# Kernel optimization log

Hardware: AMD Instinct MI355X
Metric: run time of the kernel (lower is better)

The kernel has to match this reference:

```python
import jax, jax.numpy as jnp
import numpy as np

IN_C = 31
OUT_C = 8                      # C: mean/scale channels and Givens rotation size
A_C = OUT_C * (OUT_C - 1) // 2 # 28 rotation angles
TOT = OUT_C + OUT_C + A_C      # encoder output channels = 44
SMIN, SMAX = 0.001, 1000.0
B, H, W = 4, 256, 256


def setup_inputs() -> dict:
    key = jax.random.key(0)
    k1, k2, k3 = jax.random.split(key, 3)
    x = jax.random.normal(k1, (B, IN_C, H, W), dtype=jnp.float32)
    Wenc = jax.random.normal(k2, (TOT, IN_C), dtype=jnp.float32) * (1.0 / np.sqrt(IN_C))
    benc = jax.random.normal(k3, (TOT,), dtype=jnp.float32) * 0.01
    return {"x": x, "Wenc": Wenc, "benc": benc}


def reference(x, Wenc, benc):
    C = OUT_C
    # encoder: 1x1 conv -> (B, TOT, H, W)
    w = jnp.einsum('bchw,oc->bohw', x, Wenc) + benc[None, :, None, None]
    m = jnp.transpose(w[:, :C], (0, 2, 3, 1))                 # (B,H,W,C)
    sig = jax.nn.sigmoid(w[:, C:2 * C])
    s = SMIN * (1.0 - sig) + SMAX * sig                       # (B,C,H,W)
    a = jnp.pi * jnp.tanh(w[:, 2 * C:])                       # (B,A,H,W)
    cs = jnp.cos(a)
    ss = jnp.sin(a)
    # R = prod of Givens rotations; right-multiplying by rij only updates
    # columns i and j, so we never materialize per-pair (B,H,W,C,C) identities.
    eye = jnp.eye(C, dtype=x.dtype)
    R = jnp.broadcast_to(eye, (x.shape[0], x.shape[2], x.shape[3], C, C))
    c = 0
    for i in range(C - 1):
        for j in range(i + 1, C):
            cij = cs[:, c][..., None]   # (B,H,W,1)
            sij = ss[:, c][..., None]
            col_i = R[..., i]           # (B,H,W,C)
            col_j = R[..., j]
            R = R.at[..., i].set(col_i * cij + col_j * sij)
            R = R.at[..., j].set(col_j * cij - col_i * sij)
            c += 1
    sp = jnp.transpose(s, (0, 2, 3, 1))                       # (B,H,W,C)
    # S = R^T D R with D = diag(sp), per pixel
    S = jnp.einsum('bhwji,bhwj,bhwjk->bhwik', R, sp, R)
    S = 0.5 * (S + jnp.swapaxes(S, -1, -2))
    return m, S
```

## Files before the change

kernel.cpp:

```cpp
#include <hip/hip_runtime.h>
#include <math.h>

constexpr int IN_C = 31;
constexpr int TOT  = 44;
constexpr int HW   = 256 * 256;
constexpr int NPIX = 4 * HW;
constexpr float SMIN = 0.001f, SMAX = 1000.0f;

typedef __attribute__((ext_vector_type(8))) short bf16x8;
typedef __attribute__((ext_vector_type(4))) float f32x4;

__device__ __forceinline__ float frcp(float v) { return __builtin_amdgcn_rcpf(v); }

__device__ __forceinline__ short f2bf(float f) {
    union { float f; unsigned u; } v; v.f = f;
    unsigned r = v.u + 0x7FFFu + ((v.u >> 16) & 1u);
    return (short)(r >> 16);
}
__device__ __forceinline__ float bf2f(short h) {
    union { unsigned u; float f; } v; v.u = ((unsigned)(unsigned short)h) << 16;
    return v.f;
}

__global__ __launch_bounds__(64, 4) void sepgpd_fused(
    const float* __restrict__ x,
    const float* __restrict__ Wenc,
    const float* __restrict__ benc,
    float* __restrict__ out)
{
    __shared__ float wt[64 * 34];

    const int lane = threadIdx.x;
    const int W0   = blockIdx.x * 64;
    const int b    = W0 >> 16;
    const int hwb  = W0 & (HW - 1);
    const int lrow = lane & 15;
    const int lgrp = lane >> 4;

    const float* xb = x + (size_t)b * IN_C * HW + hwb;

    bf16x8 bhi[3], blo[3];
#pragma unroll
    for (int n = 0; n < 3; ++n) {
        const int o = n * 16 + lrow;
#pragma unroll
        for (int j = 0; j < 8; ++j) {
            const int k = lgrp * 8 + j;
            const float wv = (o < TOT && k < IN_C) ? Wenc[o * IN_C + k] : 0.0f;
            const short h = f2bf(wv);
            bhi[n][j] = h;
            blo[n][j] = f2bf(wv - bf2f(h));
        }
    }

    f32x4 acc[4][3];
#pragma unroll
    for (int t = 0; t < 4; ++t)
#pragma unroll
        for (int n = 0; n < 3; ++n) acc[t][n] = (f32x4)0.0f;

#pragma unroll
    for (int t = 0; t < 4; ++t) {
        float xf[8];
#pragma unroll
        for (int j = 0; j < 8; ++j) {
            const int k = lgrp * 8 + j;
            xf[j] = (k < IN_C) ? xb[(size_t)k * HW + t * 16 + lrow] : 0.0f;
        }
        bf16x8 ahi, alo;
#pragma unroll
        for (int j = 0; j < 8; ++j) {
            const short h = f2bf(xf[j]);
            ahi[j] = h;
            alo[j] = f2bf(xf[j] - bf2f(h));
        }
#pragma unroll
        for (int n = 0; n < 3; ++n) {
            acc[t][n] = __builtin_amdgcn_mfma_f32_16x16x32_bf16(ahi, bhi[n], acc[t][n], 0, 0, 0);
            acc[t][n] = __builtin_amdgcn_mfma_f32_16x16x32_bf16(alo, bhi[n], acc[t][n], 0, 0, 0);
            acc[t][n] = __builtin_amdgcn_mfma_f32_16x16x32_bf16(ahi, blo[n], acc[t][n], 0, 0, 0);
        }
    }

#pragma unroll
    for (int t = 0; t < 4; ++t)
#pragma unroll
        for (int n = 0; n < 2; ++n)
#pragma unroll
            for (int r = 0; r < 4; ++r) {
                const int p = t * 16 + lgrp * 4 + r;
                wt[p * 34 + n * 16 + lrow] = acc[t][n][r];
            }

    float a16[16];
#pragma unroll
    for (int c = 0; c < 16; ++c) a16[c] = wt[lane * 34 + c];

    asm volatile("" ::: "memory");

#pragma unroll
    for (int t = 0; t < 4; ++t)
#pragma unroll
        for (int r = 0; r < 4; ++r) {
            const int p = t * 16 + lgrp * 4 + r;
            wt[p * 34 + lrow] = acc[t][2][r];
        }

    const int pix = W0 + lane;
    float4* mp = reinterpret_cast<float4*>(out + (size_t)pix * 8);
    mp[0] = make_float4(a16[0] + benc[0], a16[1] + benc[1],
                        a16[2] + benc[2], a16[3] + benc[3]);
    mp[1] = make_float4(a16[4] + benc[4], a16[5] + benc[5],
                        a16[6] + benc[6], a16[7] + benc[7]);

    float sq[8];
#pragma unroll
    for (int j = 0; j < 8; ++j) {
        const float sig = frcp(1.0f + __expf(-(a16[8 + j] + benc[8 + j])));
        const float s   = fmaf(SMAX - SMIN, sig, SMIN);
        sq[j] = __builtin_amdgcn_sqrtf(s);
    }

    float R[8][8];
#pragma unroll
    for (int i = 0; i < 8; ++i)
#pragma unroll
        for (int k = 0; k < 8; ++k) R[i][k] = (i == k) ? 1.0f : 0.0f;

    int cc = 0;
#pragma unroll
    for (int i = 0; i < 7; ++i) {
#pragma unroll
        for (int j = i + 1; j < 8; ++j) {
            const int  col = (cc < 16) ? (16 + cc) : (cc - 16);
            const float wv = wt[lane * 34 + col] + benc[16 + cc];
            const float th  = fmaf(-2.0f, frcp(__expf(2.0f * wv) + 1.0f), 1.0f);
            const float rev = 0.5f * th;
            const float cs  = __builtin_amdgcn_cosf(rev);
            const float ss  = __builtin_amdgcn_sinf(rev);
#pragma unroll
            for (int r = 0; r < 8; ++r) {
                const float ri = R[r][i];
                const float rj = R[r][j];
                R[r][i] = fmaf(ri, cs, rj * ss);
                R[r][j] = fmaf(rj, cs, -(ri * ss));
            }
            ++cc;
        }
    }

    asm volatile("" ::: "memory");

#pragma unroll
    for (int j = 0; j < 8; ++j)
#pragma unroll
        for (int k = 0; k < 8; ++k) R[j][k] *= sq[j];

    float4* wbuf4 = reinterpret_cast<float4*>(wt);
    float4* S4 = reinterpret_cast<float4*>(out + (size_t)NPIX * 8);
    const size_t pixbase4 = (size_t)W0 * 16;

#pragma unroll
    for (int p = 0; p < 2; ++p) {
#pragma unroll
        for (int r = 0; r < 4; ++r) {
            const int i = 4 * p + r;
            float row[8];
#pragma unroll
            for (int k = 0; k < 8; ++k) {
                float d = 0.0f;
#pragma unroll
                for (int j = 0; j < 8; ++j) d = fmaf(R[j][i], R[j][k], d);
                row[k] = d;
            }
            const int v0 = r * 2, v1 = v0 + 1;
            wbuf4[lane * 8 + (v0 ^ (lane & 7))] =
                make_float4(row[0], row[1], row[2], row[3]);
            wbuf4[lane * 8 + (v1 ^ (lane & 7))] =
                make_float4(row[4], row[5], row[6], row[7]);
        }
#pragma unroll
        for (int k = 0; k < 8; ++k) {
            const int t  = k * 64 + lane;
            const int pl = t >> 3;
            const int v  = t & 7;
            S4[pixbase4 + (size_t)pl * 16 + p * 8 + v] =
                wbuf4[pl * 8 + (v ^ (pl & 7))];
        }
    }
}

extern "C" void kernel_launch(void* const* d_in, const int* in_sizes, int n_in,
                              void* d_out, int out_size, void* d_ws, size_t ws_size,
                              hipStream_t stream)
{
    const float* x    = (const float*)d_in[0];
    const float* Wenc = (const float*)d_in[1];
    const float* benc = (const float*)d_in[2];
    float* out        = (float*)d_out;

    dim3 grid(NPIX / 64), block(64);
    sepgpd_fused<<<grid, block, 0, stream>>>(x, Wenc, benc, out);
}
```

Measured before the change: 27.24 us.

## Split fused kernel into encoder and Givens-rotation tail kernels via workspace

```diff
diff --git a/kernel.cpp b/kernel.cpp
--- a/kernel.cpp
+++ b/kernel.cpp
@@ -5,6 +5,7 @@
 constexpr int TOT  = 44;
 constexpr int HW   = 256 * 256;
 constexpr int NPIX = 4 * HW;
+constexpr int NWG  = NPIX / 64;
 constexpr float SMIN = 0.001f, SMAX = 1000.0f;
 
 typedef __attribute__((ext_vector_type(8))) short bf16x8;
@@ -20,6 +21,193 @@
 __device__ __forceinline__ float bf2f(short h) {
     union { unsigned u; float f; } v; v.u = ((unsigned)(unsigned short)h) << 16;
     return v.f;
+}
+
+__global__ __launch_bounds__(64, 4) void sepgpd_enc(
+    const float* __restrict__ x,
+    const float* __restrict__ Wenc,
+    const float* __restrict__ benc,
+    float* __restrict__ out,
+    float* __restrict__ ws)
+{
+    __shared__ float wt[64 * 34];
+
+    const int lane = threadIdx.x;
+    const int W0   = blockIdx.x * 64;
+    const int b    = W0 >> 16;
+    const int hwb  = W0 & (HW - 1);
+    const int lrow = lane & 15;
+    const int lgrp = lane >> 4;
+
+    const float* xb = x + (size_t)b * IN_C * HW + hwb;
+
+    bf16x8 bhi[3], blo[3];
+#pragma unroll
+    for (int n = 0; n < 3; ++n) {
+        const int o = n * 16 + lrow;
+#pragma unroll
+        for (int j = 0; j < 8; ++j) {
+            const int k = lgrp * 8 + j;
+            const float wv = (o < TOT && k < IN_C) ? Wenc[o * IN_C + k] : 0.0f;
+            const short h = f2bf(wv);
+            bhi[n][j] = h;
+            blo[n][j] = f2bf(wv - bf2f(h));
+        }
+    }
+
+    f32x4 acc[4][3];
+#pragma unroll
+    for (int t = 0; t < 4; ++t)
+#pragma unroll
+        for (int n = 0; n < 3; ++n) acc[t][n] = (f32x4)0.0f;
+
+#pragma unroll
+    for (int t = 0; t < 4; ++t) {
+        float xf[8];
+#pragma unroll
+        for (int j = 0; j < 8; ++j) {
+            const int k = lgrp * 8 + j;
+            xf[j] = (k < IN_C) ? xb[(size_t)k * HW + t * 16 + lrow] : 0.0f;
+        }
+        bf16x8 ahi, alo;
+#pragma unroll
+        for (int j = 0; j < 8; ++j) {
+            const short h = f2bf(xf[j]);
+            ahi[j] = h;
+            alo[j] = f2bf(xf[j] - bf2f(h));
+        }
+#pragma unroll
+        for (int n = 0; n < 3; ++n) {
+            acc[t][n] = __builtin_amdgcn_mfma_f32_16x16x32_bf16(ahi, bhi[n], acc[t][n], 0, 0, 0);
+            acc[t][n] = __builtin_amdgcn_mfma_f32_16x16x32_bf16(alo, bhi[n], acc[t][n], 0, 0, 0);
+            acc[t][n] = __builtin_amdgcn_mfma_f32_16x16x32_bf16(ahi, blo[n], acc[t][n], 0, 0, 0);
+        }
+    }
+
+#pragma unroll
+    for (int t = 0; t < 4; ++t)
+#pragma unroll
+        for (int n = 0; n < 2; ++n)
+#pragma unroll
+            for (int r = 0; r < 4; ++r) {
+                const int p = t * 16 + lgrp * 4 + r;
+                wt[p * 34 + n * 16 + lrow] = acc[t][n][r];
+            }
+
+    float a16[16];
+#pragma unroll
+    for (int c = 0; c < 16; ++c) a16[c] = wt[lane * 34 + c];
+
+    asm volatile("" ::: "memory");
+
+#pragma unroll
+    for (int t = 0; t < 4; ++t)
+#pragma unroll
+        for (int r = 0; r < 4; ++r) {
+            const int p = t * 16 + lgrp * 4 + r;
+            wt[p * 34 + lrow] = acc[t][2][r];
+        }
+
+    const int pix = W0 + lane;
+    float4* mp = reinterpret_cast<float4*>(out + (size_t)pix * 8);
+    mp[0] = make_float4(a16[0] + benc[0], a16[1] + benc[1],
+                        a16[2] + benc[2], a16[3] + benc[3]);
+    mp[1] = make_float4(a16[4] + benc[4], a16[5] + benc[5],
+                        a16[6] + benc[6], a16[7] + benc[7]);
+
+#pragma unroll
+    for (int j = 0; j < 8; ++j) {
+        const float sig = frcp(1.0f + __expf(-(a16[8 + j] + benc[8 + j])));
+        const float s   = fmaf(SMAX - SMIN, sig, SMIN);
+        ws[(size_t)j * NPIX + pix] = __builtin_amdgcn_sqrtf(s);
+    }
+
+#pragma unroll
+    for (int cc = 0; cc < 28; ++cc) {
+        const int  col = (cc < 16) ? (16 + cc) : (cc - 16);
+        const float wv = wt[lane * 34 + col] + benc[16 + cc];
+        const float th = fmaf(-2.0f, frcp(__expf(2.0f * wv) + 1.0f), 1.0f);
+        ws[(size_t)(8 + cc) * NPIX + pix] = 0.5f * th;
+    }
+}
+
+__global__ __launch_bounds__(64, 4) void sepgpd_tail(
+    const float* __restrict__ ws,
+    float* __restrict__ out)
+{
+    __shared__ float4 wbuf4[512];
+
+    const int lane = threadIdx.x;
+    const int W0   = blockIdx.x * 64;
+    const int pix  = W0 + lane;
+
+    float sq[8];
+#pragma unroll
+    for (int j = 0; j < 8; ++j) sq[j] = ws[(size_t)j * NPIX + pix];
+    float rev[28];
+#pragma unroll
+    for (int cc = 0; cc < 28; ++cc) rev[cc] = ws[(size_t)(8 + cc) * NPIX + pix];
+
+    float R[8][8];
+#pragma unroll
+    for (int i = 0; i < 8; ++i)
+#pragma unroll
+        for (int k = 0; k < 8; ++k) R[i][k] = (i == k) ? 1.0f : 0.0f;
+
+    int cc = 0;
+#pragma unroll
+    for (int i = 0; i < 7; ++i) {
+#pragma unroll
+        for (int j = i + 1; j < 8; ++j) {
+            const float cs = __builtin_amdgcn_cosf(rev[cc]);
+            const float ss = __builtin_amdgcn_sinf(rev[cc]);
+#pragma unroll
+            for (int r = 0; r < 8; ++r) {
+                const float ri = R[r][i];
+                const float rj = R[r][j];
+                R[r][i] = fmaf(ri, cs, rj * ss);
+                R[r][j] = fmaf(rj, cs, -(ri * ss));
+            }
+            ++cc;
+        }
+    }
+
+#pragma unroll
+    for (int j = 0; j < 8; ++j)
+#pragma unroll
+        for (int k = 0; k < 8; ++k) R[j][k] *= sq[j];
+
+    float4* S4 = reinterpret_cast<float4*>(out + (size_t)NPIX * 8);
+    const size_t pixbase4 = (size_t)W0 * 16;
+
+#pragma unroll
+    for (int p = 0; p < 2; ++p) {
+#pragma unroll
+        for (int r = 0; r < 4; ++r) {
+            const int i = 4 * p + r;
+            float row[8];
+#pragma unroll
+            for (int k = 0; k < 8; ++k) {
+                float d = 0.0f;
+#pragma unroll
+                for (int j = 0; j < 8; ++j) d = fmaf(R[j][i], R[j][k], d);
+                row[k] = d;
+            }
+            const int v0 = r * 2, v1 = v0 + 1;
+            wbuf4[lane * 8 + (v0 ^ (lane & 7))] =
+                make_float4(row[0], row[1], row[2], row[3]);
+            wbuf4[lane * 8 + (v1 ^ (lane & 7))] =
+                make_float4(row[4], row[5], row[6], row[7]);
+        }
+#pragma unroll
+        for (int k = 0; k < 8; ++k) {
+            const int t  = k * 64 + lane;
+            const int pl = t >> 3;
+            const int v  = t & 7;
+            S4[pixbase4 + (size_t)pl * 16 + p * 8 + v] =
+                wbuf4[pl * 8 + (v ^ (pl & 7))];
+        }
+    }
 }
 
 __global__ __launch_bounds__(64, 4) void sepgpd_fused(
@@ -199,6 +387,12 @@
     const float* benc = (const float*)d_in[2];
     float* out        = (float*)d_out;
 
-    dim3 grid(NPIX / 64), block(64);
-    sepgpd_fused<<<grid, block, 0, stream>>>(x, Wenc, benc, out);
-}
+    const size_t need = (size_t)NPIX * 36 * sizeof(float);
+    if (ws_size >= need) {
+        float* ws = (float*)d_ws;
+        sepgpd_enc <<<dim3(NWG), dim3(64), 0, stream>>>(x, Wenc, benc, out, ws);
+        sepgpd_tail<<<dim3(NWG), dim3(64), 0, stream>>>(ws, out);
+    } else {
+        sepgpd_fused<<<dim3(NWG), dim3(64), 0, stream>>>(x, Wenc, benc, out);
+    }
+}
```

Measured after the change: 39.81 us. 1.46x slower.
